# Performance work log

Hardware: AMD Instinct MI355X
Metric: run time of the kernel (lower is better)

## Reference

```python
import jax, jax.numpy as jnp
import numpy as np

N_NODES, N_EDGES, BATCH = 50000, 100000, 256
H = 64            # dim_hidden_features
D_NODE, D_EDGE, D_RBF = 110, 8, 8
D_SET = 2 * H     # Set2Set input_dim = 128, output_dim = 256
D_HID = 512
D_CAT = 54
MP_STEPS, S2S_ITERS = 4, 3


def setup_inputs() -> dict:
    key = jax.random.key(0)
    ks = iter(jax.random.split(key, 48))

    def nrm(shape, s=0.05):
        return jax.random.normal(next(ks), shape, dtype=jnp.float32) * s

    inp = {}
    inp["node_attribute"] = jax.random.normal(next(ks), (N_NODES, D_NODE), dtype=jnp.float32)
    inp["edge_attribute"] = jax.random.normal(next(ks), (N_EDGES, D_EDGE), dtype=jnp.float32)
    inp["edge_length"] = jax.random.uniform(next(ks), (N_EDGES,), dtype=jnp.float32)
    inp["src"] = jax.random.randint(next(ks), (N_EDGES,), 0, N_NODES, dtype=jnp.int32)
    inp["dst"] = jax.random.randint(next(ks), (N_EDGES,), 0, N_NODES, dtype=jnp.int32)
    inp["node_graph"] = jnp.sort(jax.random.randint(next(ks), (N_NODES,), 0, BATCH, dtype=jnp.int32))
    # atom_feature_projector
    inp["proj_W"] = nrm((D_NODE, H)); inp["proj_b"] = jnp.zeros((H,), jnp.float32)
    # RBF layer: centers ~ U(0,1), beta = 10 (per reset_parameters)
    inp["centers"] = jax.random.uniform(next(ks), (D_RBF,), dtype=jnp.float32)
    inp["beta"] = jnp.full((D_RBF,), 10.0, jnp.float32)
    # NNConv edge function: Linear(16 -> 64*64), plus NNConv bias
    inp["bond_W"] = nrm((D_EDGE + D_RBF, H * H)); inp["bond_b"] = jnp.zeros((H * H,), jnp.float32)
    inp["conv_b"] = jnp.zeros((H,), jnp.float32)
    # GRU (input H, hidden H); PyTorch layout (3H, in)
    inp["gru_Wih"] = nrm((3 * H, H)); inp["gru_Whh"] = nrm((3 * H, H))
    inp["gru_bih"] = jnp.zeros((3 * H,), jnp.float32); inp["gru_bhh"] = jnp.zeros((3 * H,), jnp.float32)
    # Set2Set LSTM: input 2*D_SET=256, hidden D_SET=128, 2 layers; PyTorch layout (4H, in)
    inp["lstm_Wih0"] = nrm((4 * D_SET, 2 * D_SET)); inp["lstm_Whh0"] = nrm((4 * D_SET, D_SET))
    inp["lstm_bih0"] = jnp.zeros((4 * D_SET,), jnp.float32); inp["lstm_bhh0"] = jnp.zeros((4 * D_SET,), jnp.float32)
    inp["lstm_Wih1"] = nrm((4 * D_SET, D_SET)); inp["lstm_Whh1"] = nrm((4 * D_SET, D_SET))
    inp["lstm_bih1"] = jnp.zeros((4 * D_SET,), jnp.float32); inp["lstm_bhh1"] = jnp.zeros((4 * D_SET,), jnp.float32)
    # sparsify: Linear(256 -> 512) + PReLU(init 0.25)
    inp["sp_W"] = nrm((2 * D_SET, D_HID)); inp["sp_b"] = jnp.zeros((D_HID,), jnp.float32)
    inp["prelu_a"] = jnp.array([0.25], jnp.float32)
    # catalyst1 head: hiddens[0] (512->512 ReLU, 512->512 Tanh) then outputs[0] (512->54)
    inp["h0_W1"] = nrm((D_HID, D_HID)); inp["h0_b1"] = jnp.zeros((D_HID,), jnp.float32)
    inp["h0_W2"] = nrm((D_HID, D_HID)); inp["h0_b2"] = jnp.zeros((D_HID,), jnp.float32)
    inp["out_W"] = nrm((D_HID, D_CAT)); inp["out_b"] = jnp.zeros((D_CAT,), jnp.float32)
    return inp


def _lstm_cell(x, h, c, Wih, Whh, bih, bhh):
    # PyTorch LSTM gate order: i, f, g, o
    g = x @ Wih.T + bih + h @ Whh.T + bhh
    i, f, gg, o = jnp.split(g, 4, axis=-1)
    c = jax.nn.sigmoid(f) * c + jax.nn.sigmoid(i) * jnp.tanh(gg)
    h = jax.nn.sigmoid(o) * jnp.tanh(c)
    return h, c


def reference(node_attribute, edge_attribute, edge_length, src, dst, node_graph,
              proj_W, proj_b, centers, beta, bond_W, bond_b, conv_b,
              gru_Wih, gru_Whh, gru_bih, gru_bhh,
              lstm_Wih0, lstm_Whh0, lstm_bih0, lstm_bhh0,
              lstm_Wih1, lstm_Whh1, lstm_bih1, lstm_bhh1,
              sp_W, sp_b, prelu_a, h0_W1, h0_b1, h0_W2, h0_b2, out_W, out_b):
    n_nodes = node_attribute.shape[0]
    # atom feature projection
    x = jax.nn.relu(node_attribute @ proj_W + proj_b)                       # (N, H)
    # edge features = [edge_attribute, RBF(length)]
    rbf = jnp.exp(-beta * (edge_length[:, None] - centers[None, :]) ** 2)   # (E, 8)
    efeat = jnp.concatenate([edge_attribute, rbf], axis=-1)                 # (E, 16)
    # NNConv per-edge weight matrix; edge features are constant over MP steps
    W_e = (efeat @ bond_W + bond_b).reshape(-1, H, H)                       # (E, H, H)

    feat, h = x, x
    for _ in range(MP_STEPS):
        # NNConv: message = h_src @ W_e, sum-aggregated at dst, plus bias
        m = jnp.einsum('ei,eio->eo', feat[src], W_e)                        # (E, H)
        agg = jax.ops.segment_sum(m, dst, num_segments=n_nodes) + conv_b    # (N, H)
        gx = jax.nn.relu(agg)
        # GRU cell (PyTorch gate order r, z, n)
        gi = gx @ gru_Wih.T + gru_bih
        gh = h @ gru_Whh.T + gru_bhh
        i_r, i_z, i_n = jnp.split(gi, 3, axis=-1)
        h_r, h_z, h_n = jnp.split(gh, 3, axis=-1)
        r = jax.nn.sigmoid(i_r + h_r)
        z = jax.nn.sigmoid(i_z + h_z)
        n = jnp.tanh(i_n + r * h_n)
        h = (1.0 - z) * n + z * h
        feat = h
    node_agg = jnp.concatenate([feat, x], axis=-1)                          # (N, 2H)

    # Set2Set pooling over graphs (segment softmax attention, 2-layer LSTM)
    B = BATCH
    h0 = c0 = jnp.zeros((B, D_SET), node_agg.dtype)
    h1 = c1 = jnp.zeros((B, D_SET), node_agg.dtype)
    q_star = jnp.zeros((B, 2 * D_SET), node_agg.dtype)
    for _ in range(S2S_ITERS):
        h0, c0 = _lstm_cell(q_star, h0, c0, lstm_Wih0, lstm_Whh0, lstm_bih0, lstm_bhh0)
        h1, c1 = _lstm_cell(h0, h1, c1, lstm_Wih1, lstm_Whh1, lstm_bih1, lstm_bhh1)
        q = h1                                                              # (B, 128)
        e = jnp.sum(node_agg * q[node_graph], axis=-1)                      # (N,)
        emax = jax.ops.segment_max(e, node_graph, num_segments=B)
        p = jnp.exp(e - emax[node_graph])
        denom = jax.ops.segment_sum(p, node_graph, num_segments=B)
        alpha = p / denom[node_graph]                                       # per-graph softmax
        r_out = jax.ops.segment_sum(node_agg * alpha[:, None], node_graph, num_segments=B)
        q_star = jnp.concatenate([q, r_out], axis=-1)                       # (B, 256)

    # sparsify (Linear + PReLU)
    feats = q_star @ sp_W + sp_b                                            # (B, 512)
    feats = jnp.where(feats >= 0, feats, prelu_a * feats)
    # catalyst1 head
    hid = jnp.tanh(jax.nn.relu(feats @ h0_W1 + h0_b1) @ h0_W2 + h0_b2)
    return jax.nn.softmax(hid @ out_W + out_b, axis=-1)                     # (B, 54)
```

## Files before the change

kernel.cpp:

```cpp
#include <hip/hip_runtime.h>
#include <math.h>

constexpr int N = 50000;
constexpr int E = 100000;
constexpr int B = 256;
constexpr int H = 64;
constexpr int DN = 110;

#define DEV __device__ __forceinline__

typedef __attribute__((ext_vector_type(8))) short short8;
typedef __attribute__((ext_vector_type(4))) float floatx4;

DEV float sigf(float x) { return 1.0f / (1.0f + expf(-x)); }

DEV short f2bf(float f) {
    unsigned u = __float_as_uint(f);
    unsigned r = (u + 0x7fffu + ((u >> 16) & 1u)) >> 16;
    return (short)r;
}
DEV float bf2f(short s) { return __uint_as_float(((unsigned)(unsigned short)s) << 16); }

DEV void cvt8(const float* p, short8& hi, short8& lo) {
    float4 u0 = *(const float4*)p;
    float4 u1 = *(const float4*)(p + 4);
    float vv[8] = {u0.x, u0.y, u0.z, u0.w, u1.x, u1.y, u1.z, u1.w};
#pragma unroll
    for (int j = 0; j < 8; ++j) {
        short hb = f2bf(vv[j]);
        hi[j] = hb;
        lo[j] = f2bf(vv[j] - bf2f(hb));
    }
}

__global__ void k_izero(int* p, int n) {
    int i = blockIdx.x * 256 + threadIdx.x;
    if (i < n) p[i] = 0;
}

DEV void d_transpose(const float* in, float* out, int R, int C, int idx) {
    int r = idx / C, c = idx % C;
    out[c * R + r] = in[idx];
}

DEV void d_prepB(const float* __restrict__ W, short* __restrict__ out,
                 int NT16, int ld, int trans, int ocap, int idx) {
    int lane = idx & 63;
    int t = idx >> 6;
    int ntile = t % NT16;
    int kt = t / NT16;
    int quad = lane >> 4, col = lane & 15;
    int o = ntile * 16 + col;
    short hi[8], lo[8];
#pragma unroll
    for (int j = 0; j < 8; ++j) {
        int k = kt * 32 + quad * 8 + j;
        float v = 0.0f;
        if (o < ocap) v = trans ? W[(size_t)o * ld + k] : W[(size_t)k * ld + o];
        short hb = f2bf(v);
        hi[j] = hb;
        lo[j] = f2bf(v - bf2f(hb));
    }
    short* dh = out + (((size_t)(t * 2 + 0) * 64 + lane) * 8);
    short* dl = out + (((size_t)(t * 2 + 1) * 64 + lane) * 8);
#pragma unroll
    for (int j = 0; j < 8; ++j) { dh[j] = hi[j]; dl[j] = lo[j]; }
}

DEV void d_prepW(const float* __restrict__ bond_W, const float* __restrict__ bond_b,
                 short* __restrict__ wf, int idx) {
    int lane = idx & 63;
    int t = idx >> 6;
    int ks = t & 1;
    int nt = (t >> 1) & 3;
    int kk = t >> 3;
    const float* S = (kk < 16) ? (bond_W + kk * 4096) : bond_b;
    int quad = lane >> 4, col = lane & 15;
    short hi[8], lo[8];
#pragma unroll
    for (int j = 0; j < 8; ++j) {
        int i = ks * 32 + quad * 8 + j;
        float v = S[i * 64 + nt * 16 + col];
        short hb = f2bf(v);
        hi[j] = hb;
        lo[j] = f2bf(v - bf2f(hb));
    }
    short* dh = wf + (((size_t)(t * 2 + 0) * 64 + lane) * 8);
    short* dl = wf + (((size_t)(t * 2 + 1) * 64 + lane) * 8);
#pragma unroll
    for (int j = 0; j < 8; ++j) { dh[j] = hi[j]; dl[j] = lo[j]; }
}

__launch_bounds__(256)
__global__ void k_prep0(const float* lWih0, const float* lWhh0, const float* lWih1, const float* lWhh1,
                        float* lW0T, float* lU0T, float* lW1T, float* lU1T,
                        const float* bond_W, const float* bond_b, short* wf,
                        const float* gru_Wih, const float* gru_Whh, short* fgI, short* fgH,
                        float* zreg) {
    int idx = blockIdx.x * 256 + threadIdx.x;
    if (idx < 131072) { d_transpose(lWih0, lW0T, 512, 256, idx); return; }
    idx -= 131072;
    if (idx < 65536) { d_transpose(lWhh0, lU0T, 512, 128, idx); return; }
    idx -= 65536;
    if (idx < 65536) { d_transpose(lWih1, lW1T, 512, 128, idx); return; }
    idx -= 65536;
    if (idx < 65536) { d_transpose(lWhh1, lU1T, 512, 128, idx); return; }
    idx -= 65536;
    if (idx < 8704) { d_prepW(bond_W, bond_b, wf, idx); return; }
    idx -= 8704;
    if (idx < 1536) { d_prepB(gru_Wih, fgI, 12, 64, 1, 192, idx); return; }
    idx -= 1536;
    if (idx < 1536) { d_prepB(gru_Whh, fgH, 12, 64, 1, 192, idx); return; }
    idx -= 1536;
    if (idx < 196608) { zreg[idx] = 0.0f; return; }
}
constexpr int PREP0_TOTAL = 131072 + 3 * 65536 + 8704 + 2 * 1536 + 196608;

__launch_bounds__(256)
__global__ void k_prephead(const float* sp_W, short* fsp, const float* h0_W1, short* fw1,
                           const float* h0_W2, short* fw2, const float* out_W, short* fow) {
    int idx = blockIdx.x * 256 + threadIdx.x;
    if (idx < 16384) { d_prepB(sp_W, fsp, 32, 512, 0, 512, idx); return; }
    idx -= 16384;
    if (idx < 32768) { d_prepB(h0_W1, fw1, 32, 512, 0, 512, idx); return; }
    idx -= 32768;
    if (idx < 32768) { d_prepB(h0_W2, fw2, 32, 512, 0, 512, idx); return; }
    idx -= 32768;
    if (idx < 4096) { d_prepB(out_W, fow, 4, 54, 0, 54, idx); return; }
}
constexpr int PREPH_TOTAL = 16384 + 2 * 32768 + 4096;

__global__ void k_deg(const int* __restrict__ dst, int* __restrict__ deg) {
    int e = blockIdx.x * 256 + threadIdx.x;
    if (e < E) atomicAdd(&deg[dst[e]], 1);
}
__global__ void k_scan1(const int* __restrict__ deg, int* __restrict__ bsum) {
    __shared__ int s[256];
    int b = blockIdx.x, tid = threadIdx.x;
    int idx = b * 256 + tid;
    s[tid] = (idx < N) ? deg[idx] : 0;
    __syncthreads();
    for (int st = 128; st > 0; st >>= 1) {
        if (tid < st) s[tid] += s[tid + st];
        __syncthreads();
    }
    if (tid == 0) bsum[b] = s[0];
}
__global__ void k_scan2p(int* __restrict__ bsum, int nb) {
    __shared__ int s[256];
    int tid = threadIdx.x;
    int v = (tid < nb) ? bsum[tid] : 0;
    s[tid] = v;
    __syncthreads();
    for (int off = 1; off < 256; off <<= 1) {
        int t = (tid >= off) ? s[tid - off] : 0;
        __syncthreads();
        s[tid] += t;
        __syncthreads();
    }
    if (tid < nb) bsum[tid] = s[tid] - v;
}
__global__ void k_scan3(const int* __restrict__ deg, const int* __restrict__ bsum,
                        int* __restrict__ cursor, int* __restrict__ roff) {
    __shared__ int s[256];
    int b = blockIdx.x, tid = threadIdx.x;
    int idx = b * 256 + tid;
    int v = (idx < N) ? deg[idx] : 0;
    s[tid] = v;
    __syncthreads();
    for (int off = 1; off < 256; off <<= 1) {
        int t = (tid >= off) ? s[tid - off] : 0;
        __syncthreads();
        s[tid] += t;
        __syncthreads();
    }
    if (idx < N) {
        int start = bsum[b] + s[tid] - v;
        cursor[idx] = start;
        roff[idx] = start;
    }
    if (idx == 0) roff[N] = E;
}
__global__ void k_scat(const int* __restrict__ src, const int* __restrict__ dst,
                       int* __restrict__ cursor, int* __restrict__ srcp,
                       int* __restrict__ epos) {
    int e = blockIdx.x * 256 + threadIdx.x;
    if (e >= E) return;
    int d = dst[e];
    int pos = atomicAdd(&cursor[d], 1);
    srcp[pos] = src[e];
    epos[e] = pos;
}

__launch_bounds__(256)
__global__ void k_proj(const float* __restrict__ na, const float* __restrict__ W,
                       const float* __restrict__ b, float* __restrict__ x,
                       short* __restrict__ hs) {
    __shared__ float Ws[DN * 64];
    __shared__ float as[16][112];
    int tid = threadIdx.x;
    for (int i = tid; i < DN * 64; i += 256) Ws[i] = W[i];
    int n0 = blockIdx.x * 16;
    for (int i = tid; i < 16 * DN; i += 256) {
        int nn = i / DN, ii = i % DN;
        as[nn][ii] = na[(n0 + nn) * DN + ii];
    }
    __syncthreads();
    int o = tid & 63, ng = tid >> 6;
    float bo = b[o];
    for (int j = 0; j < 4; ++j) {
        int nn = ng * 4 + j;
        float acc = bo;
#pragma unroll 10
        for (int i = 0; i < DN; ++i) acc += as[nn][i] * Ws[i * 64 + o];
        float v = fmaxf(acc, 0.0f);
        int n = n0 + nn;
        x[(size_t)n * 64 + o] = v;
        short hb = f2bf(v);
        hs[(size_t)n * 128 + o] = hb;
        hs[(size_t)n * 128 + 64 + o] = f2bf(v - bf2f(hb));
    }
}

__global__ void k_efeat2(const float* __restrict__ ea, const float* __restrict__ el,
                         const float* __restrict__ centers, const float* __restrict__ beta,
                         const int* __restrict__ epos, float* __restrict__ ef_t) {
    int e = blockIdx.x * 256 + threadIdx.x;
    if (e >= E) return;
    int pos = epos[e];
    float L = el[e];
#pragma unroll
    for (int j = 0; j < 8; ++j) ef_t[j * E + pos] = ea[e * 8 + j];
#pragma unroll
    for (int j = 0; j < 8; ++j) {
        float d = L - centers[j];
        ef_t[(8 + j) * E + pos] = expf(-beta[j] * d * d);
    }
    ef_t[16 * E + pos] = 1.0f;
}

__launch_bounds__(256)
__global__ void k_msg8(const short* __restrict__ hs, const float* __restrict__ ef_t,
                       const short* __restrict__ wf, const int* __restrict__ srcp,
                       float* __restrict__ m) {
    __shared__ float efs[17 * 64];
    __shared__ int srcs[64];

    int tid = threadIdx.x;
    int e0 = blockIdx.x * 64;
    int lane = tid & 63;
    int nt = tid >> 6;
    int quad = lane >> 4, col = lane & 15;

    if (tid < 64) {
        int eg = e0 + tid;
        srcs[tid] = (eg < E) ? srcp[eg] : 0;
    }
    for (int i = tid; i < 17 * 64; i += 256) {
        int kk = i >> 6, e = i & 63;
        int eg = e0 + e;
        efs[i] = (eg < E) ? ef_t[(size_t)kk * E + eg] : 0.0f;
    }
    __syncthreads();

    short8 Ah[4][2], Al[4][2];
#pragma unroll
    for (int mt = 0; mt < 4; ++mt) {
        int s = srcs[mt * 16 + col];
        const short* hp = hs + (size_t)s * 128 + quad * 8;
#pragma unroll
        for (int ks = 0; ks < 2; ++ks) {
            Ah[mt][ks] = *(const short8*)(hp + ks * 32);
            Al[mt][ks] = *(const short8*)(hp + 64 + ks * 32);
        }
    }

    const short8* Wf = (const short8*)wf;
    float C[4][4] = {};

#define LOADB(d0, d1, d2, d3, KK)                      \
    {                                                  \
        int tb_ = ((KK) * 4 + nt) * 2;                 \
        d0 = Wf[((tb_ + 0) * 2 + 0) * 64 + lane];      \
        d1 = Wf[((tb_ + 1) * 2 + 0) * 64 + lane];      \
        d2 = Wf[((tb_ + 0) * 2 + 1) * 64 + lane];      \
        d3 = Wf[((tb_ + 1) * 2 + 1) * 64 + lane];      \
    }

    short8 c0, c1, c2, c3, n0_, n1_, n2_, n3_, q0, q1, q2, q3;
    LOADB(c0, c1, c2, c3, 0);
    LOADB(n0_, n1_, n2_, n3_, 1);
    LOADB(q0, q1, q2, q3, 2);

#pragma unroll 1
    for (int kk = 0; kk < 17; ++kk) {
        int kn = kk + 3;
        if (kn > 16) kn = 16;
        short8 p0, p1, p2, p3;
        LOADB(p0, p1, p2, p3, kn);

#pragma unroll
        for (int mt = 0; mt < 4; ++mt) {
            floatx4 T = {0.0f, 0.0f, 0.0f, 0.0f};
            T = __builtin_amdgcn_mfma_f32_16x16x32_bf16(Ah[mt][0], c0, T, 0, 0, 0);
            T = __builtin_amdgcn_mfma_f32_16x16x32_bf16(Ah[mt][1], c1, T, 0, 0, 0);
            T = __builtin_amdgcn_mfma_f32_16x16x32_bf16(Al[mt][0], c0, T, 0, 0, 0);
            T = __builtin_amdgcn_mfma_f32_16x16x32_bf16(Al[mt][1], c1, T, 0, 0, 0);
            T = __builtin_amdgcn_mfma_f32_16x16x32_bf16(Ah[mt][0], c2, T, 0, 0, 0);
            T = __builtin_amdgcn_mfma_f32_16x16x32_bf16(Ah[mt][1], c3, T, 0, 0, 0);
            float4 ef = *(const float4*)&efs[kk * 64 + mt * 16 + quad * 4];
            C[mt][0] += ef.x * T[0];
            C[mt][1] += ef.y * T[1];
            C[mt][2] += ef.z * T[2];
            C[mt][3] += ef.w * T[3];
        }
        c0 = n0_; c1 = n1_; c2 = n2_; c3 = n3_;
        n0_ = q0; n1_ = q1; n2_ = q2; n3_ = q3;
        q0 = p0; q1 = p1; q2 = p2; q3 = p3;
    }
#undef LOADB

    int o = nt * 16 + col;
#pragma unroll
    for (int mt = 0; mt < 4; ++mt) {
#pragma unroll
        for (int r = 0; r < 4; ++r) {
            int eg = e0 + mt * 16 + quad * 4 + r;
            if (eg < E) m[(size_t)eg * 64 + o] = C[mt][r];
        }
    }
}

__launch_bounds__(256)
__global__ void k_gru3(const float* __restrict__ m, const int* __restrict__ roff,
                       const float* __restrict__ conv_b, short* __restrict__ hs,
                       const short* __restrict__ fI, const short* __restrict__ fH,
                       const float* __restrict__ bih, const float* __restrict__ bhh) {
    int tid = threadIdx.x, lane = tid & 63, nt = tid >> 6;
    int quad = lane >> 4, col = lane & 15;
    int n0 = blockIdx.x * 32;

    short8 Gh[2][2], Gl[2][2], Hh[2][2], Hl[2][2];
#pragma unroll
    for (int mt = 0; mt < 2; ++mt) {
        int node = n0 + mt * 16 + col;
        bool ok = node < N;
        int nc = ok ? node : (N - 1);
        int rs = roff[nc];
        int re = ok ? roff[nc + 1] : rs;
        float acc[2][8];
#pragma unroll
        for (int ks = 0; ks < 2; ++ks) {
            const float* cb = conv_b + ks * 32 + quad * 8;
#pragma unroll
            for (int j = 0; j < 8; ++j) acc[ks][j] = cb[j];
        }
        for (int r = rs; r < re; ++r) {
            const float* mp = m + (size_t)r * 64 + quad * 8;
            float4 a0 = *(const float4*)mp;
            float4 a1 = *(const float4*)(mp + 4);
            float4 b0 = *(const float4*)(mp + 32);
            float4 b1 = *(const float4*)(mp + 36);
            acc[0][0] += a0.x; acc[0][1] += a0.y; acc[0][2] += a0.z; acc[0][3] += a0.w;
            acc[0][4] += a1.x; acc[0][5] += a1.y; acc[0][6] += a1.z; acc[0][7] += a1.w;
            acc[1][0] += b0.x; acc[1][1] += b0.y; acc[1][2] += b0.z; acc[1][3] += b0.w;
            acc[1][4] += b1.x; acc[1][5] += b1.y; acc[1][6] += b1.z; acc[1][7] += b1.w;
        }
        const short* hp = hs + (size_t)nc * 128 + quad * 8;
#pragma unroll
        for (int ks = 0; ks < 2; ++ks) {
            short8 hh8 = *(const short8*)(hp + ks * 32);
            short8 hl8 = *(const short8*)(hp + 64 + ks * 32);
            Hh[mt][ks] = hh8;
            Hl[mt][ks] = hl8;
#pragma unroll
            for (int j = 0; j < 8; ++j) {
                float g = ok ? fmaxf(acc[ks][j], 0.0f) : 0.0f;
                short gb = f2bf(g);
                Gh[mt][ks][j] = gb;
                Gl[mt][ks][j] = f2bf(g - bf2f(gb));
            }
        }
        if (!ok) {
#pragma unroll
            for (int ks = 0; ks < 2; ++ks) {
                Hh[mt][ks] = short8{0,0,0,0,0,0,0,0};
                Hl[mt][ks] = short8{0,0,0,0,0,0,0,0};
            }
        }
    }
    __syncthreads();

    const short8* FI = (const short8*)fI;
    const short8* FH = (const short8*)fH;
    floatx4 aI[2][3] = {}, aH[2][3] = {};
#pragma unroll
    for (int ks = 0; ks < 2; ++ks) {
        short8 bIh[3], bIl[3], bHh[3], bHl[3];
#pragma unroll
        for (int g = 0; g < 3; ++g) {
            int t = ks * 12 + g * 4 + nt;
            bIh[g] = FI[(t * 2 + 0) * 64 + lane];
            bIl[g] = FI[(t * 2 + 1) * 64 + lane];
            bHh[g] = FH[(t * 2 + 0) * 64 + lane];
            bHl[g] = FH[(t * 2 + 1) * 64 + lane];
        }
#pragma unroll
        for (int mt = 0; mt < 2; ++mt) {
#pragma unroll
            for (int g = 0; g < 3; ++g) {
                aI[mt][g] = __builtin_amdgcn_mfma_f32_16x16x32_bf16(Gh[mt][ks], bIh[g], aI[mt][g], 0, 0, 0);
                aI[mt][g] = __builtin_amdgcn_mfma_f32_16x16x32_bf16(Gl[mt][ks], bIh[g], aI[mt][g], 0, 0, 0);
                aI[mt][g] = __builtin_amdgcn_mfma_f32_16x16x32_bf16(Gh[mt][ks], bIl[g], aI[mt][g], 0, 0, 0);
                aH[mt][g] = __builtin_amdgcn_mfma_f32_16x16x32_bf16(Hh[mt][ks], bHh[g], aH[mt][g], 0, 0, 0);
                aH[mt][g] = __builtin_amdgcn_mfma_f32_16x16x32_bf16(Hl[mt][ks], bHh[g], aH[mt][g], 0, 0, 0);
                aH[mt][g] = __builtin_amdgcn_mfma_f32_16x16x32_bf16(Hh[mt][ks], bHl[g], aH[mt][g], 0, 0, 0);
            }
        }
    }

    int o = nt * 16 + col;
    float br = bih[o], bz = bih[64 + o], bn = bih[128 + o];
    float cr = bhh[o], cz = bhh[64 + o], cn = bhh[128 + o];
#pragma unroll
    for (int mt = 0; mt < 2; ++mt) {
#pragma unroll
        for (int r = 0; r < 4; ++r) {
            int node = n0 + mt * 16 + quad * 4 + r;
            if (node >= N) continue;
            float rg = sigf(aI[mt][0][r] + br + aH[mt][0][r] + cr);
            float z  = sigf(aI[mt][1][r] + bz + aH[mt][1][r] + cz);
            float ng = tanhf(aI[mt][2][r] + bn + rg * (aH[mt][2][r] + cn));
            size_t hb_ = (size_t)node * 128 + o;
            float hold = bf2f(hs[hb_]) + bf2f(hs[hb_ + 64]);
            float hn = (1.0f - z) * ng + z * hold;
            short hi = f2bf(hn);
            hs[hb_] = hi;
            hs[hb_ + 64] = f2bf(hn - bf2f(hi));
        }
    }
}

__global__ void k_bounds2(const int* __restrict__ ng, int* __restrict__ gs, int* __restrict__ ge) {
    int n = blockIdx.x * 256 + threadIdx.x;
    if (n >= N) return;
    int g = ng[n];
    int gp = (n == 0) ? -1 : ng[n - 1];
    if (g != gp) {
        gs[g] = n;
        if (n > 0) ge[gp] = n;
        for (int q = gp + 1; q < g; ++q) { gs[q] = 0; ge[q] = 0; }
    }
    if (n == N - 1) {
        ge[g] = N;
        for (int q = g + 1; q < B; ++q) { gs[q] = 0; ge[q] = 0; }
    }
}

__launch_bounds__(256)
__global__ void k_s2s(float* __restrict__ h0, float* __restrict__ c0,
                      float* __restrict__ h1, float* __restrict__ c1,
                      float* __restrict__ q_star,
                      const float* __restrict__ W0T, const float* __restrict__ U0T,
                      const float* __restrict__ b0i, const float* __restrict__ b0h,
                      const float* __restrict__ W1T, const float* __restrict__ U1T,
                      const float* __restrict__ b1i, const float* __restrict__ b1h,
                      const short* __restrict__ hs, const float* __restrict__ x,
                      const int* __restrict__ gs, const int* __restrict__ ge) {
    __shared__ float xb[256], hb[128], gb[512], h0n[128], qv[128];
    __shared__ float mrg[4][2][64];
    __shared__ float ml[4][2];
    int g = blockIdx.x, tid = threadIdx.x;
    xb[tid] = q_star[g * 256 + tid];
    if (tid < 128) hb[tid] = h0[g * 128 + tid];
    __syncthreads();
    float g0 = b0i[tid] + b0h[tid];
    float g1 = b0i[tid + 256] + b0h[tid + 256];
    for (int i = 0; i < 256; ++i) {
        float xx = xb[i];
        g0 += xx * W0T[i * 512 + tid];
        g1 += xx * W0T[i * 512 + tid + 256];
    }
    for (int i = 0; i < 128; ++i) {
        float hh = hb[i];
        g0 += hh * U0T[i * 512 + tid];
        g1 += hh * U0T[i * 512 + tid + 256];
    }
    gb[tid] = g0; gb[tid + 256] = g1;
    __syncthreads();
    if (tid < 128) {
        float ii = gb[tid], ff = gb[128 + tid], gg = gb[256 + tid], oo = gb[384 + tid];
        float c = sigf(ff) * c0[g * 128 + tid] + sigf(ii) * tanhf(gg);
        float hn = sigf(oo) * tanhf(c);
        c0[g * 128 + tid] = c; h0[g * 128 + tid] = hn; h0n[tid] = hn;
        hb[tid] = h1[g * 128 + tid];
    }
    __syncthreads();
    float ga = b1i[tid] + b1h[tid];
    float gbv = b1i[tid + 256] + b1h[tid + 256];
    for (int i = 0; i < 128; ++i) {
        float xx = h0n[i], hh = hb[i];
        ga  += xx * W1T[i * 512 + tid]       + hh * U1T[i * 512 + tid];
        gbv += xx * W1T[i * 512 + tid + 256] + hh * U1T[i * 512 + tid + 256];
    }
    gb[tid] = ga; gb[tid + 256] = gbv;
    __syncthreads();
    if (tid < 128) {
        float ii = gb[tid], ff = gb[128 + tid], gg = gb[256 + tid], oo = gb[384 + tid];
        float c = sigf(ff) * c1[g * 128 + tid] + sigf(ii) * tanhf(gg);
        float hn = sigf(oo) * tanhf(c);
        c1[g * 128 + tid] = c; h1[g * 128 + tid] = hn;
        q_star[g * 256 + tid] = hn;
        qv[tid] = hn;
    }
    __syncthreads();
    int s0v = gs[g], s1v = ge[g];
    int lane = tid & 63, grp = tid >> 6;
    float qh = qv[lane], qx = qv[64 + lane];
    float mM = -INFINITY, lL = 0.0f, nh = 0.0f, nx = 0.0f;
    for (int n = s0v + grp; n < s1v; n += 16) {
        float hv[4], xv[4], e[4];
#pragma unroll
        for (int j = 0; j < 4; ++j) {
            int nj = n + 4 * j;
            int nc = (nj < s1v) ? nj : n;
            hv[j] = bf2f(hs[(size_t)nc * 128 + lane]) + bf2f(hs[(size_t)nc * 128 + 64 + lane]);
            xv[j] = x[(size_t)nc * 64 + lane];
            e[j] = hv[j] * qh + xv[j] * qx;
        }
#pragma unroll
        for (int off = 32; off; off >>= 1) {
#pragma unroll
            for (int j = 0; j < 4; ++j) e[j] += __shfl_xor(e[j], off, 64);
        }
#pragma unroll
        for (int j = 0; j < 4; ++j)
            if (n + 4 * j >= s1v) e[j] = -INFINITY;
        float mb = fmaxf(fmaxf(e[0], e[1]), fmaxf(e[2], e[3]));
        float mn = fmaxf(mM, mb);
        float sc = expf(mM - mn);
        float w0 = expf(e[0] - mn), w1 = expf(e[1] - mn);
        float w2 = expf(e[2] - mn), w3 = expf(e[3] - mn);
        lL = lL * sc + ((w0 + w1) + (w2 + w3));
        nh = nh * sc + ((w0 * hv[0] + w1 * hv[1]) + (w2 * hv[2] + w3 * hv[3]));
        nx = nx * sc + ((w0 * xv[0] + w1 * xv[1]) + (w2 * xv[2] + w3 * xv[3]));
        mM = mn;
    }
    mrg[grp][0][lane] = nh;
    mrg[grp][1][lane] = nx;
    if (lane == 0) { ml[grp][0] = mM; ml[grp][1] = lL; }
    __syncthreads();
    if (tid < 128) {
        int half = tid >> 6, dl = tid & 63;
        float M = -INFINITY;
#pragma unroll
        for (int i = 0; i < 4; ++i) M = fmaxf(M, ml[i][0]);
        float L = 0.0f, NUM = 0.0f;
#pragma unroll
        for (int i = 0; i < 4; ++i) {
            float sc = expf(ml[i][0] - M);
            L += ml[i][1] * sc;
            NUM += mrg[i][half][dl] * sc;
        }
        q_star[g * 256 + 128 + tid] = (s1v > s0v) ? NUM / L : 0.0f;
    }
}

template<int MODE>
__launch_bounds__(256)
__global__ void k_hgemm(const float* __restrict__ A, const short* __restrict__ Bf,
                        const float* __restrict__ bias, const float* __restrict__ pa,
                        float* __restrict__ Cout, int K, int NT16) {
    int tid = threadIdx.x, lane = tid & 63, nt = tid >> 6;
    int quad = lane >> 4, col = lane & 15;
    int s0 = blockIdx.x * 16;
    int ntile = blockIdx.y * 4 + nt;
    int NoutTot = NT16 * 16;
    const short8* F = (const short8*)Bf;
    floatx4 T = {0.0f, 0.0f, 0.0f, 0.0f};
    const float* ap = A + (size_t)(s0 + col) * K + quad * 8;
    int KT = K >> 5;
#pragma unroll 4
    for (int kt = 0; kt < KT; ++kt) {
        short8 ah, al;
        cvt8(ap + kt * 32, ah, al);
        int t = kt * NT16 + ntile;
        short8 bh = F[(t * 2 + 0) * 64 + lane];
        short8 bl = F[(t * 2 + 1) * 64 + lane];
        T = __builtin_amdgcn_mfma_f32_16x16x32_bf16(ah, bh, T, 0, 0, 0);
        T = __builtin_amdgcn_mfma_f32_16x16x32_bf16(al, bh, T, 0, 0, 0);
        T = __builtin_amdgcn_mfma_f32_16x16x32_bf16(ah, bl, T, 0, 0, 0);
    }
    int o = ntile * 16 + col;
    float b = bias[o];
    float a = (MODE == 0) ? pa[0] : 0.0f;
#pragma unroll
    for (int r = 0; r < 4; ++r) {
        float v = T[r] + b;
        if (MODE == 0) v = (v >= 0.0f) ? v : a * v;
        if (MODE == 1) v = fmaxf(v, 0.0f);
        if (MODE == 2) v = tanhf(v);
        Cout[(size_t)(s0 + quad * 4 + r) * NoutTot + o] = v;
    }
}

__launch_bounds__(256)
__global__ void k_hout(const float* __restrict__ A, const short* __restrict__ Bf,
                       const float* __restrict__ ob, float* __restrict__ out) {
    __shared__ float sm[16][64];
    __shared__ float smax[16], sinv[16];
    int tid = threadIdx.x, lane = tid & 63, nt = tid >> 6;
    int quad = lane >> 4, col = lane & 15;
    int s0 = blockIdx.x * 16;
    const short8* F = (const short8*)Bf;
    floatx4 T = {0.0f, 0.0f, 0.0f, 0.0f};
    const float* ap = A + (size_t)(s0 + col) * 512 + quad * 8;
#pragma unroll 4
    for (int kt = 0; kt < 16; ++kt) {
        short8 ah, al;
        cvt8(ap + kt * 32, ah, al);
        int t = kt * 4 + nt;
        short8 bh = F[(t * 2 + 0) * 64 + lane];
        short8 bl = F[(t * 2 + 1) * 64 + lane];
        T = __builtin_amdgcn_mfma_f32_16x16x32_bf16(ah, bh, T, 0, 0, 0);
        T = __builtin_amdgcn_mfma_f32_16x16x32_bf16(al, bh, T, 0, 0, 0);
        T = __builtin_amdgcn_mfma_f32_16x16x32_bf16(ah, bl, T, 0, 0, 0);
    }
    int o = nt * 16 + col;
    float b = (o < 54) ? ob[o] : 0.0f;
#pragma unroll
    for (int r = 0; r < 4; ++r)
        sm[quad * 4 + r][o] = (o < 54) ? (T[r] + b) : -1e30f;
    __syncthreads();
    if (tid < 16) {
        float m = -INFINITY;
        for (int j = 0; j < 54; ++j) m = fmaxf(m, sm[tid][j]);
        float s = 0.0f;
        for (int j = 0; j < 54; ++j) s += expf(sm[tid][j] - m);
        smax[tid] = m;
        sinv[tid] = 1.0f / s;
    }
    __syncthreads();
    for (int idx = tid; idx < 16 * 54; idx += 256) {
        int srow = idx / 54, oo = idx % 54;
        out[(size_t)(s0 + srow) * 54 + oo] = expf(sm[srow][oo] - smax[srow]) * sinv[srow];
    }
}

extern "C" void kernel_launch(void* const* d_in, const int* in_sizes, int n_in,
                              void* d_out, int out_size, void* d_ws, size_t ws_size,
                              hipStream_t stream) {
    const float* node_attr = (const float*)d_in[0];
    const float* edge_attr = (const float*)d_in[1];
    const float* edge_len  = (const float*)d_in[2];
    const int*   src       = (const int*)d_in[3];
    const int*   dst       = (const int*)d_in[4];
    const int*   node_grph = (const int*)d_in[5];
    const float* proj_W    = (const float*)d_in[6];
    const float* proj_b    = (const float*)d_in[7];
    const float* centers   = (const float*)d_in[8];
    const float* beta      = (const float*)d_in[9];
    const float* bond_W    = (const float*)d_in[10];
    const float* bond_b    = (const float*)d_in[11];
    const float* conv_b    = (const float*)d_in[12];
    const float* gru_Wih   = (const float*)d_in[13];
    const float* gru_Whh   = (const float*)d_in[14];
    const float* gru_bih   = (const float*)d_in[15];
    const float* gru_bhh   = (const float*)d_in[16];
    const float* lWih0     = (const float*)d_in[17];
    const float* lWhh0     = (const float*)d_in[18];
    const float* lbih0     = (const float*)d_in[19];
    const float* lbhh0     = (const float*)d_in[20];
    const float* lWih1     = (const float*)d_in[21];
    const float* lWhh1     = (const float*)d_in[22];
    const float* lbih1     = (const float*)d_in[23];
    const float* lbhh1     = (const float*)d_in[24];
    const float* sp_W      = (const float*)d_in[25];
    const float* sp_b      = (const float*)d_in[26];
    const float* prelu_a   = (const float*)d_in[27];
    const float* h0_W1     = (const float*)d_in[28];
    const float* h0_b1     = (const float*)d_in[29];
    const float* h0_W2     = (const float*)d_in[30];
    const float* h0_b2     = (const float*)d_in[31];
    const float* out_W     = (const float*)d_in[32];
    const float* out_b     = (const float*)d_in[33];
    float* out = (float*)d_out;

    float* ws = (float*)d_ws;
    size_t off = 0;
    float* x      = ws + off; off += (size_t)N * 64;
    float* hsf    = ws + off; off += (size_t)N * 64;
    float* ef_t   = ws + off; off += (size_t)E * 17;
    float* m      = ws + off; off += (size_t)E * 64;
    float* wfrag  = ws + off; off += 17 * 16 * 64 * 8 / 2;
    float* fgI    = ws + off; off += 2 * 64 * 192 / 2;
    float* fgH    = ws + off; off += 2 * 64 * 192 / 2;
    float* lW0T   = ws + off; off += 256 * 512;
    float* lU0T   = ws + off; off += 128 * 512;
    float* lW1T   = ws + off; off += 128 * 512;
    float* lU1T   = ws + off; off += 128 * 512;
    float* h0     = ws + off; off += B * 128;
    float* c0     = ws + off; off += B * 128;
    float* h1     = ws + off; off += B * 128;
    float* c1     = ws + off; off += B * 128;
    float* q_star = ws + off; off += B * 256;
    int* gs       = (int*)(ws + off); off += B;
    int* ge       = (int*)(ws + off); off += B;
    int* deg      = (int*)(ws + off); off += N;
    int* cursor   = (int*)(ws + off); off += N;
    int* roff     = (int*)(ws + off); off += N + 1;
    int* bsum     = (int*)(ws + off); off += 256;
    int* srcp     = (int*)(ws + off); off += E;
    int* epos     = (int*)(ws + off); off += E;

    short* hs = (short*)hsf;

    short* fsp = (short*)ef_t;
    short* fw1 = (short*)(ef_t + 131072);
    short* fw2 = (short*)(ef_t + 131072 + 262144);
    short* fow = (short*)(ef_t + 131072 + 2 * 262144);
    float* hb1 = ef_t + 131072 + 2 * 262144 + 32768;
    float* hb2 = hb1 + 131072;

    constexpr int NB = (N + 255) / 256;

    k_izero<<<NB, 256, 0, stream>>>(deg, N);
    k_deg<<<(E + 255) / 256, 256, 0, stream>>>(dst, deg);
    k_scan1<<<NB, 256, 0, stream>>>(deg, bsum);
    k_scan2p<<<1, 256, 0, stream>>>(bsum, NB);
    k_scan3<<<NB, 256, 0, stream>>>(deg, bsum, cursor, roff);
    k_scat<<<(E + 255) / 256, 256, 0, stream>>>(src, dst, cursor, srcp, epos);

    k_prep0<<<(PREP0_TOTAL + 255) / 256, 256, 0, stream>>>(
        lWih0, lWhh0, lWih1, lWhh1, lW0T, lU0T, lW1T, lU1T,
        bond_W, bond_b, (short*)wfrag, gru_Wih, gru_Whh, (short*)fgI, (short*)fgH, h0);

    k_proj<<<N / 16, 256, 0, stream>>>(node_attr, proj_W, proj_b, x, hs);
    k_efeat2<<<(E + 255) / 256, 256, 0, stream>>>(edge_attr, edge_len, centers, beta, epos, ef_t);

    k_bounds2<<<(N + 255) / 256, 256, 0, stream>>>(node_grph, gs, ge);

    for (int step = 0; step < 4; ++step) {
        k_msg8<<<(E + 63) / 64, 256, 0, stream>>>(hs, ef_t, (const short*)wfrag, srcp, m);
        k_gru3<<<(N + 31) / 32, 256, 0, stream>>>(m, roff, conv_b, hs,
                                                  (const short*)fgI, (const short*)fgH,
                                                  gru_bih, gru_bhh);
    }

    k_prephead<<<(PREPH_TOTAL + 255) / 256, 256, 0, stream>>>(
        sp_W, fsp, h0_W1, fw1, h0_W2, fw2, out_W, fow);

    for (int it = 0; it < 3; ++it) {
        k_s2s<<<B, 256, 0, stream>>>(h0, c0, h1, c1, q_star,
                                     lW0T, lU0T, lbih0, lbhh0,
                                     lW1T, lU1T, lbih1, lbhh1,
                                     hs, x, gs, ge);
    }

    k_hgemm<0><<<dim3(16, 8), 256, 0, stream>>>(q_star, fsp, sp_b, prelu_a, hb1, 256, 32);
    k_hgemm<1><<<dim3(16, 8), 256, 0, stream>>>(hb1, fw1, h0_b1, nullptr, hb2, 512, 32);
    k_hgemm<2><<<dim3(16, 8), 256, 0, stream>>>(hb2, fw2, h0_b2, nullptr, hb1, 512, 32);
    k_hout<<<16, 256, 0, stream>>>(hb1, fow, out_b, out);
}
```

Baseline: 781.8 us.

## Fuse per-destination message aggregation into message kernel and use MFMA for projection

The message kernel now reduces its 64 dst-sorted edge messages per block into per-node sums in shared memory. It writes those sums directly to an N×64 aggregate buffer, and writes a per-block partial sum for nodes whose edge runs cross block boundaries. The GRU kernel reads one aggregate row plus any boundary partials instead of looping over E×64 message rows, so far less message data moves through global memory. The node projection also switches to split-bf16 MFMA using a prepacked weight fragment. The cost is a serial 64-step scan by one wave per block and more complex handling of nodes that span blocks.

```diff
diff --git a/kernel.cpp b/kernel.cpp
--- a/kernel.cpp
+++ b/kernel.cpp
@@ -6,6 +6,7 @@
 constexpr int B = 256;
 constexpr int H = 64;
 constexpr int DN = 110;
+constexpr int NBLK = (E + 63) / 64;
 
 #define DEV __device__ __forceinline__
 
@@ -44,7 +45,7 @@
 }
 
 DEV void d_prepB(const float* __restrict__ W, short* __restrict__ out,
-                 int NT16, int ld, int trans, int ocap, int idx) {
+                 int NT16, int ld, int trans, int ocap, int kcap, int idx) {
     int lane = idx & 63;
     int t = idx >> 6;
     int ntile = t % NT16;
@@ -56,7 +57,7 @@
     for (int j = 0; j < 8; ++j) {
         int k = kt * 32 + quad * 8 + j;
         float v = 0.0f;
-        if (o < ocap) v = trans ? W[(size_t)o * ld + k] : W[(size_t)k * ld + o];
+        if (o < ocap && k < kcap) v = trans ? W[(size_t)o * ld + k] : W[(size_t)k * ld + o];
         short hb = f2bf(v);
         hi[j] = hb;
         lo[j] = f2bf(v - bf2f(hb));
@@ -96,6 +97,7 @@
                         float* lW0T, float* lU0T, float* lW1T, float* lU1T,
                         const float* bond_W, const float* bond_b, short* wf,
                         const float* gru_Wih, const float* gru_Whh, short* fgI, short* fgH,
+                        const float* proj_W, short* fproj,
                         float* zreg) {
     int idx = blockIdx.x * 256 + threadIdx.x;
     if (idx < 131072) { d_transpose(lWih0, lW0T, 512, 256, idx); return; }
@@ -108,25 +110,27 @@
     idx -= 65536;
     if (idx < 8704) { d_prepW(bond_W, bond_b, wf, idx); return; }
     idx -= 8704;
-    if (idx < 1536) { d_prepB(gru_Wih, fgI, 12, 64, 1, 192, idx); return; }
+    if (idx < 1536) { d_prepB(gru_Wih, fgI, 12, 64, 1, 192, 64, idx); return; }
     idx -= 1536;
-    if (idx < 1536) { d_prepB(gru_Whh, fgH, 12, 64, 1, 192, idx); return; }
+    if (idx < 1536) { d_prepB(gru_Whh, fgH, 12, 64, 1, 192, 64, idx); return; }
     idx -= 1536;
+    if (idx < 1024) { d_prepB(proj_W, fproj, 4, 64, 0, 64, DN, idx); return; }
+    idx -= 1024;
     if (idx < 196608) { zreg[idx] = 0.0f; return; }
 }
-constexpr int PREP0_TOTAL = 131072 + 3 * 65536 + 8704 + 2 * 1536 + 196608;
+constexpr int PREP0_TOTAL = 131072 + 3 * 65536 + 8704 + 2 * 1536 + 1024 + 196608;
 
 __launch_bounds__(256)
 __global__ void k_prephead(const float* sp_W, short* fsp, const float* h0_W1, short* fw1,
                            const float* h0_W2, short* fw2, const float* out_W, short* fow) {
     int idx = blockIdx.x * 256 + threadIdx.x;
-    if (idx < 16384) { d_prepB(sp_W, fsp, 32, 512, 0, 512, idx); return; }
+    if (idx < 16384) { d_prepB(sp_W, fsp, 32, 512, 0, 512, 256, idx); return; }
     idx -= 16384;
-    if (idx < 32768) { d_prepB(h0_W1, fw1, 32, 512, 0, 512, idx); return; }
+    if (idx < 32768) { d_prepB(h0_W1, fw1, 32, 512, 0, 512, 512, idx); return; }
     idx -= 32768;
-    if (idx < 32768) { d_prepB(h0_W2, fw2, 32, 512, 0, 512, idx); return; }
+    if (idx < 32768) { d_prepB(h0_W2, fw2, 32, 512, 0, 512, 512, idx); return; }
     idx -= 32768;
-    if (idx < 4096) { d_prepB(out_W, fow, 4, 54, 0, 54, idx); return; }
+    if (idx < 4096) { d_prepB(out_W, fow, 4, 54, 0, 54, 512, idx); return; }
 }
 constexpr int PREPH_TOTAL = 16384 + 2 * 32768 + 4096;
 
@@ -183,38 +187,59 @@
 }
 __global__ void k_scat(const int* __restrict__ src, const int* __restrict__ dst,
                        int* __restrict__ cursor, int* __restrict__ srcp,
-                       int* __restrict__ epos) {
+                       int* __restrict__ epos, int* __restrict__ dstp) {
     int e = blockIdx.x * 256 + threadIdx.x;
     if (e >= E) return;
     int d = dst[e];
     int pos = atomicAdd(&cursor[d], 1);
     srcp[pos] = src[e];
+    dstp[pos] = d;
     epos[e] = pos;
 }
 
 __launch_bounds__(256)
-__global__ void k_proj(const float* __restrict__ na, const float* __restrict__ W,
-                       const float* __restrict__ b, float* __restrict__ x,
-                       short* __restrict__ hs) {
-    __shared__ float Ws[DN * 64];
-    __shared__ float as[16][112];
-    int tid = threadIdx.x;
-    for (int i = tid; i < DN * 64; i += 256) Ws[i] = W[i];
-    int n0 = blockIdx.x * 16;
+__global__ void k_projm(const float* __restrict__ na, const short* __restrict__ fp,
+                        const float* __restrict__ b, float* __restrict__ x,
+                        short* __restrict__ hs) {
+    __shared__ float as[16 * 132];
+    int tid = threadIdx.x, lane = tid & 63, nt = tid >> 6;
+    int quad = lane >> 4, col = lane & 15;
+    int s0 = blockIdx.x * 16;
     for (int i = tid; i < 16 * DN; i += 256) {
-        int nn = i / DN, ii = i % DN;
-        as[nn][ii] = na[(n0 + nn) * DN + ii];
-    }
-    __syncthreads();
-    int o = tid & 63, ng = tid >> 6;
+        int r = i / DN, c = i % DN;
+        as[r * 132 + c] = na[(size_t)s0 * DN + i];
+    }
+    for (int i = tid; i < 16 * 22; i += 256) {
+        int r = i / 22, c = DN + i % 22;
+        as[r * 132 + c] = 0.0f;
+    }
+    __syncthreads();
+    const short8* F = (const short8*)fp;
+    floatx4 T = {0.0f, 0.0f, 0.0f, 0.0f};
+#pragma unroll
+    for (int kt = 0; kt < 4; ++kt) {
+        const float* ap = as + col * 132 + kt * 32 + quad * 8;
+        short8 ah, al;
+#pragma unroll
+        for (int j = 0; j < 8; ++j) {
+            float v = ap[j];
+            short hb = f2bf(v);
+            ah[j] = hb;
+            al[j] = f2bf(v - bf2f(hb));
+        }
+        int t = kt * 4 + nt;
+        short8 bh = F[(t * 2 + 0) * 64 + lane];
+        short8 bl = F[(t * 2 + 1) * 64 + lane];
+        T = __builtin_amdgcn_mfma_f32_16x16x32_bf16(ah, bh, T, 0, 0, 0);
+        T = __builtin_amdgcn_mfma_f32_16x16x32_bf16(al, bh, T, 0, 0, 0);
+        T = __builtin_amdgcn_mfma_f32_16x16x32_bf16(ah, bl, T, 0, 0, 0);
+    }
+    int o = nt * 16 + col;
     float bo = b[o];
-    for (int j = 0; j < 4; ++j) {
-        int nn = ng * 4 + j;
-        float acc = bo;
-#pragma unroll 10
-        for (int i = 0; i < DN; ++i) acc += as[nn][i] * Ws[i * 64 + o];
-        float v = fmaxf(acc, 0.0f);
-        int n = n0 + nn;
+#pragma unroll
+    for (int r = 0; r < 4; ++r) {
+        int n = s0 + quad * 4 + r;
+        float v = fmaxf(T[r] + bo, 0.0f);
         x[(size_t)n * 64 + o] = v;
         short hb = f2bf(v);
         hs[(size_t)n * 128 + o] = hb;
@@ -240,11 +265,15 @@
 }
 
 __launch_bounds__(256)
-__global__ void k_msg8(const short* __restrict__ hs, const float* __restrict__ ef_t,
-                       const short* __restrict__ wf, const int* __restrict__ srcp,
-                       float* __restrict__ m) {
+__global__ void k_msgagg(const short* __restrict__ hs, const float* __restrict__ ef_t,
+                         const short* __restrict__ wf, const int* __restrict__ srcp,
+                         const int* __restrict__ dstp,
+                         float* __restrict__ agg, float* __restrict__ bpart) {
     __shared__ float efs[17 * 64];
     __shared__ int srcs[64];
+    __shared__ int dsh[64];
+    __shared__ int shprev;
+    __shared__ float Csh[64][65];
 
     int tid = threadIdx.x;
     int e0 = blockIdx.x * 64;
@@ -255,7 +284,9 @@
     if (tid < 64) {
         int eg = e0 + tid;
         srcs[tid] = (eg < E) ? srcp[eg] : 0;
-    }
+        dsh[tid] = (eg < E) ? dstp[eg] : N;
+    }
+    if (tid == 0) shprev = (e0 == 0) ? -1 : dstp[e0 - 1];
     for (int i = tid; i < 17 * 64; i += 256) {
         int kk = i >> 6, e = i & 63;
         int eg = e0 + e;
@@ -320,20 +351,47 @@
     }
 #undef LOADB
 
-    int o = nt * 16 + col;
-#pragma unroll
-    for (int mt = 0; mt < 4; ++mt) {
-#pragma unroll
-        for (int r = 0; r < 4; ++r) {
-            int eg = e0 + mt * 16 + quad * 4 + r;
-            if (eg < E) m[(size_t)eg * 64 + o] = C[mt][r];
+#pragma unroll
+    for (int mt = 0; mt < 4; ++mt)
+#pragma unroll
+        for (int r = 0; r < 4; ++r)
+            Csh[mt * 16 + quad * 4 + r][nt * 16 + col] = C[mt][r];
+    __syncthreads();
+
+    if (tid < 64) {
+        int c = tid;
+        int prevd = shprev;
+        int firstd = dsh[0];
+        for (int q = prevd + 1; q < firstd; ++q) agg[(size_t)q * 64 + c] = 0.0f;
+        int cur = firstd;
+        float acc = 0.0f;
+        bool owned = (e0 == 0) || (firstd != prevd);
+        bool done = false;
+        for (int r = 0; r < 64; ++r) {
+            int d = dsh[r];
+            if (d != cur) {
+                if (owned) agg[(size_t)cur * 64 + c] = acc;
+                else bpart[(size_t)blockIdx.x * 64 + c] = acc;
+                int dc = (d < N) ? d : N;
+                for (int q = cur + 1; q < dc; ++q) agg[(size_t)q * 64 + c] = 0.0f;
+                cur = d;
+                acc = 0.0f;
+                owned = true;
+                if (cur >= N) { done = true; break; }
+            }
+            acc += Csh[r][c];
+        }
+        if (!done) {
+            if (owned) agg[(size_t)cur * 64 + c] = acc;
+            else bpart[(size_t)blockIdx.x * 64 + c] = acc;
         }
     }
 }
 
 __launch_bounds__(256)
-__global__ void k_gru3(const float* __restrict__ m, const int* __restrict__ roff,
-                       const float* __restrict__ conv_b, short* __restrict__ hs,
+__global__ void k_gru4(const float* __restrict__ agg, const float* __restrict__ bpart,
+                       const int* __restrict__ roff, const float* __restrict__ conv_b,
+                       short* __restrict__ hs,
                        const short* __restrict__ fI, const short* __restrict__ fH,
                        const float* __restrict__ bih, const float* __restrict__ bhh) {
     int tid = threadIdx.x, lane = tid & 63, nt = tid >> 6;
@@ -346,25 +404,34 @@
         int node = n0 + mt * 16 + col;
         bool ok = node < N;
         int nc = ok ? node : (N - 1);
-        int rs = roff[nc];
-        int re = ok ? roff[nc + 1] : rs;
         float acc[2][8];
+        const float* ag = agg + (size_t)nc * 64;
 #pragma unroll
         for (int ks = 0; ks < 2; ++ks) {
             const float* cb = conv_b + ks * 32 + quad * 8;
-#pragma unroll
-            for (int j = 0; j < 8; ++j) acc[ks][j] = cb[j];
-        }
-        for (int r = rs; r < re; ++r) {
-            const float* mp = m + (size_t)r * 64 + quad * 8;
-            float4 a0 = *(const float4*)mp;
-            float4 a1 = *(const float4*)(mp + 4);
-            float4 b0 = *(const float4*)(mp + 32);
-            float4 b1 = *(const float4*)(mp + 36);
-            acc[0][0] += a0.x; acc[0][1] += a0.y; acc[0][2] += a0.z; acc[0][3] += a0.w;
-            acc[0][4] += a1.x; acc[0][5] += a1.y; acc[0][6] += a1.z; acc[0][7] += a1.w;
-            acc[1][0] += b0.x; acc[1][1] += b0.y; acc[1][2] += b0.z; acc[1][3] += b0.w;
-            acc[1][4] += b1.x; acc[1][5] += b1.y; acc[1][6] += b1.z; acc[1][7] += b1.w;
+            float4 a0 = *(const float4*)(ag + ks * 32 + quad * 8);
+            float4 a1 = *(const float4*)(ag + ks * 32 + quad * 8 + 4);
+            acc[ks][0] = a0.x + cb[0]; acc[ks][1] = a0.y + cb[1];
+            acc[ks][2] = a0.z + cb[2]; acc[ks][3] = a0.w + cb[3];
+            acc[ks][4] = a1.x + cb[4]; acc[ks][5] = a1.y + cb[5];
+            acc[ks][6] = a1.z + cb[6]; acc[ks][7] = a1.w + cb[7];
+        }
+        int rs = roff[nc];
+        int re = roff[nc + 1];
+        if (re > rs) {
+            int b0 = rs >> 6, b1 = (re - 1) >> 6;
+            for (int bb = b0 + 1; bb <= b1; ++bb) {
+                const float* bp = bpart + (size_t)bb * 64;
+#pragma unroll
+                for (int ks = 0; ks < 2; ++ks) {
+                    float4 p0 = *(const float4*)(bp + ks * 32 + quad * 8);
+                    float4 p1 = *(const float4*)(bp + ks * 32 + quad * 8 + 4);
+                    acc[ks][0] += p0.x; acc[ks][1] += p0.y;
+                    acc[ks][2] += p0.z; acc[ks][3] += p0.w;
+                    acc[ks][4] += p1.x; acc[ks][5] += p1.y;
+                    acc[ks][6] += p1.z; acc[ks][7] += p1.w;
+                }
+            }
         }
         const short* hp = hs + (size_t)nc * 128 + quad * 8;
 #pragma unroll
@@ -691,10 +758,11 @@
     float* x      = ws + off; off += (size_t)N * 64;
     float* hsf    = ws + off; off += (size_t)N * 64;
     float* ef_t   = ws + off; off += (size_t)E * 17;
-    float* m      = ws + off; off += (size_t)E * 64;
+    float* agg    = ws + off; off += (size_t)N * 64;
     float* wfrag  = ws + off; off += 17 * 16 * 64 * 8 / 2;
     float* fgI    = ws + off; off += 2 * 64 * 192 / 2;
     float* fgH    = ws + off; off += 2 * 64 * 192 / 2;
+    float* fproj  = ws + off; off += 16 * 1024 / 2;
     float* lW0T   = ws + off; off += 256 * 512;
     float* lU0T   = ws + off; off += 128 * 512;
     float* lW1T   = ws + off; off += 128 * 512;
@@ -704,6 +772,7 @@
     float* h1     = ws + off; off += B * 128;
     float* c1     = ws + off; off += B * 128;
     float* q_star = ws + off; off += B * 256;
+    float* bpart  = ws + off; off += (size_t)NBLK * 64;
     int* gs       = (int*)(ws + off); off += B;
     int* ge       = (int*)(ws + off); off += B;
     int* deg      = (int*)(ws + off); off += N;
@@ -712,6 +781,7 @@
     int* bsum     = (int*)(ws + off); off += 256;
     int* srcp     = (int*)(ws + off); off += E;
     int* epos     = (int*)(ws + off); off += E;
+    int* dstp     = (int*)(ws + off); off += E;
 
     short* hs = (short*)hsf;
 
@@ -729,20 +799,22 @@
     k_scan1<<<NB, 256, 0, stream>>>(deg, bsum);
     k_scan2p<<<1, 256, 0, stream>>>(bsum, NB);
     k_scan3<<<NB, 256, 0, stream>>>(deg, bsum, cursor, roff);
-    k_scat<<<(E + 255) / 256, 256, 0, stream>>>(src, dst, cursor, srcp, epos);
+    k_scat<<<(E + 255) / 256, 256, 0, stream>>>(src, dst, cursor, srcp, epos, dstp);
 
     k_prep0<<<(PREP0_TOTAL + 255) / 256, 256, 0, stream>>>(
         lWih0, lWhh0, lWih1, lWhh1, lW0T, lU0T, lW1T, lU1T,
-        bond_W, bond_b, (short*)wfrag, gru_Wih, gru_Whh, (short*)fgI, (short*)fgH, h0);
-
-    k_proj<<<N / 16, 256, 0, stream>>>(node_attr, proj_W, proj_b, x, hs);
+        bond_W, bond_b, (short*)wfrag, gru_Wih, gru_Whh, (short*)fgI, (short*)fgH,
+        proj_W, (short*)fproj, h0);
+
+    k_projm<<<N / 16, 256, 0, stream>>>(node_attr, (const short*)fproj, proj_b, x, hs);
     k_efeat2<<<(E + 255) / 256, 256, 0, stream>>>(edge_attr, edge_len, centers, beta, epos, ef_t);
 
     k_bounds2<<<(N + 255) / 256, 256, 0, stream>>>(node_grph, gs, ge);
 
     for (int step = 0; step < 4; ++step) {
-        k_msg8<<<(E + 63) / 64, 256, 0, stream>>>(hs, ef_t, (const short*)wfrag, srcp, m);
-        k_gru3<<<(N + 31) / 32, 256, 0, stream>>>(m, roff, conv_b, hs,
+        k_msgagg<<<NBLK, 256, 0, stream>>>(hs, ef_t, (const short*)wfrag, srcp, dstp,
+                                           agg, bpart);
+        k_gru4<<<(N + 31) / 32, 256, 0, stream>>>(agg, bpart, roff, conv_b, hs,
                                                   (const short*)fgI, (const short*)fgH,
                                                   gru_bih, gru_bhh);
     }
```

After: 734.7 us. -6.0%, faster.
